# Kernel optimization log

Measured on AMD Instinct MI355X. Metric: run time of the kernel, lower is better.

## Reference

```python
import jax, jax.numpy as jnp
import numpy as np

V = 32000   # src and trg vocab
E = 512     # embed_dim
H = 1024    # hidden_dim
S = 512     # source length
T = 512     # target length


def _lstm_scan(x_seq, h0, c0, Wih, Whh, bih, bhh):
    """Single-layer LSTM over x_seq [L, E] with PyTorch gate order (i,f,g,o)."""
    def step(carry, x):
        h, c = carry
        gates = x @ Wih.T + bih + h @ Whh.T + bhh  # [4H]
        i, f, g, o = jnp.split(gates, 4)
        i = jax.nn.sigmoid(i)
        f = jax.nn.sigmoid(f)
        g = jnp.tanh(g)
        o = jax.nn.sigmoid(o)
        c = f * c + i * g
        h = o * jnp.tanh(c)
        return (h, c), h
    (h, c), hs = jax.lax.scan(step, (h0, c0), x_seq)
    return hs, (h, c)


def setup_inputs() -> dict:
    key = jax.random.key(0)
    ks = jax.random.split(key, 16)
    s = 0.05
    return {
        "source": jax.random.randint(ks[0], (S,), 0, V),
        "target": jax.random.randint(ks[1], (T,), 0, V),
        # encoder params (embed init uniform(-0.25, 0.25) per source)
        "enc_embed": jax.random.uniform(ks[2], (V, E), jnp.float32, -0.25, 0.25),
        "enc_Wih": jax.random.normal(ks[3], (4 * H, E), jnp.float32) * s,
        "enc_Whh": jax.random.normal(ks[4], (4 * H, H), jnp.float32) * s,
        "enc_bih": jnp.zeros((4 * H,), jnp.float32),
        "enc_bhh": jnp.zeros((4 * H,), jnp.float32),
        # decoder params
        "dec_embed": jax.random.normal(ks[5], (V, E), jnp.float32) * s,
        "dec_Wih": jax.random.normal(ks[6], (4 * H, E), jnp.float32) * s,
        "dec_Whh": jax.random.normal(ks[7], (4 * H, H), jnp.float32) * s,
        "dec_bih": jnp.zeros((4 * H,), jnp.float32),
        "dec_bhh": jnp.zeros((4 * H,), jnp.float32),
        "Wout": jax.random.normal(ks[8], (V, H), jnp.float32) * s,
        "bout": jnp.zeros((V,), jnp.float32),
    }


def reference(source, target, enc_embed, enc_Wih, enc_Whh, enc_bih, enc_bhh,
              dec_embed, dec_Wih, dec_Whh, dec_bih, dec_bhh, Wout, bout):
    # ---- encoder: embed source, run LSTM from zero state, take last h ----
    src_emb = enc_embed[source]                       # [S, E]
    h0 = jnp.zeros((H,), src_emb.dtype)
    c0 = jnp.zeros((H,), src_emb.dtype)
    _, (enc_h, _) = _lstm_scan(src_emb, h0, c0, enc_Wih, enc_Whh, enc_bih, enc_bhh)
    # hidden = (enc_h, tanh(enc_h)) as in original forward
    dh0, dc0 = enc_h, jnp.tanh(enc_h)
    # ---- decoder: teacher-forced over target tokens ----
    trg_emb = dec_embed[target]                       # [T, E]
    hs, _ = _lstm_scan(trg_emb, dh0, dc0, dec_Wih, dec_Whh, dec_bih, dec_bhh)  # [T, H]
    logits = hs @ Wout.T + bout                       # [T, V]
    logp = jax.nn.log_softmax(logits, axis=-1)
    # per-step CrossEntropyLoss(output, target[i]) -> list of T scalar losses
    losses = -jnp.take_along_axis(logp, target[:, None], axis=1)[:, 0]  # [T]
    return losses
```

## Files before the change

### kernel.cpp

```cpp
#include <hip/hip_runtime.h>
#include <cstdint>
#include <cstddef>

#define V_ 32000
#define E_ 512
#define H_ 1024
#define S_ 512
#define T_ 512
#define G4 4096

typedef unsigned long long u64;

__device__ __forceinline__ float sigm(float x) { return 1.0f / (1.0f + expf(-x)); }

__global__ __launch_bounds__(256) void xi_gemm(
    const float* __restrict__ emb, const int* __restrict__ tok,
    const float* __restrict__ Wih, const float* __restrict__ b1,
    const float* __restrict__ b2, float* __restrict__ Xi) {
  __shared__ float As[32][68];
  __shared__ float Bs[32][68];
  __shared__ int ids[64];
  const int tid = threadIdx.x;
  const int tx = tid & 15, ty = tid >> 4;
  const int t0 = blockIdx.y * 64, r0 = blockIdx.x * 64;
  if (tid < 64) ids[tid] = tok[t0 + tid];
  __syncthreads();
  const int lrow = tid >> 2;
  const int lk   = (tid & 3) * 8;
  const long arow = (long)ids[lrow] * E_;
  const long brow = (long)(r0 + lrow) * E_;
  float acc[4][4] = {};
  for (int k0 = 0; k0 < E_; k0 += 32) {
    float4 a0 = *(const float4*)(emb + arow + k0 + lk);
    float4 a1 = *(const float4*)(emb + arow + k0 + lk + 4);
    float4 w0 = *(const float4*)(Wih + brow + k0 + lk);
    float4 w1 = *(const float4*)(Wih + brow + k0 + lk + 4);
    __syncthreads();
    As[lk + 0][lrow] = a0.x; As[lk + 1][lrow] = a0.y; As[lk + 2][lrow] = a0.z; As[lk + 3][lrow] = a0.w;
    As[lk + 4][lrow] = a1.x; As[lk + 5][lrow] = a1.y; As[lk + 6][lrow] = a1.z; As[lk + 7][lrow] = a1.w;
    Bs[lk + 0][lrow] = w0.x; Bs[lk + 1][lrow] = w0.y; Bs[lk + 2][lrow] = w0.z; Bs[lk + 3][lrow] = w0.w;
    Bs[lk + 4][lrow] = w1.x; Bs[lk + 5][lrow] = w1.y; Bs[lk + 6][lrow] = w1.z; Bs[lk + 7][lrow] = w1.w;
    __syncthreads();
#pragma unroll
    for (int kk = 0; kk < 32; ++kk) {
      float4 av = *(const float4*)&As[kk][ty * 4];
      float4 bv = *(const float4*)&Bs[kk][tx * 4];
      float a_[4] = {av.x, av.y, av.z, av.w};
      float b_[4] = {bv.x, bv.y, bv.z, bv.w};
#pragma unroll
      for (int i = 0; i < 4; ++i)
#pragma unroll
        for (int j = 0; j < 4; ++j) acc[i][j] += a_[i] * b_[j];
    }
  }
#pragma unroll
  for (int i = 0; i < 4; ++i) {
    const int t = t0 + ty * 4 + i;
#pragma unroll
    for (int j = 0; j < 4; ++j) {
      const int r = r0 + tx * 4 + j;
      Xi[(size_t)t * G4 + r] = acc[i][j] + b1[r] + b2[r];
    }
  }
}

__global__ __launch_bounds__(1024, 4) void lstm_seq(
    const float* __restrict__ Xi_enc, const float* __restrict__ Xi_dec,
    const float* __restrict__ Whh_enc, const float* __restrict__ Whh_dec,
    u64* __restrict__ hpair,
    float* __restrict__ hs) {
  __shared__ float h_lds[16 * 68 + 4];
  __shared__ float gates_lds[64];
  const int tid = threadIdx.x;
  const int wg = blockIdx.x;
  const int r = tid >> 4;
  const int c = tid & 15;
  const int gate = r >> 4, uu = r & 15;
  const int grow = gate * H_ + wg * 16 + uu;
  const int c64 = c * 64;

  float4 w[16];
  {
    const float* wp = Whh_enc + (size_t)grow * H_ + c64;
#pragma unroll
    for (int q = 0; q < 16; ++q) w[q] = *(const float4*)(wp + q * 4);
  }
  const float* Xi = Xi_enc;
  float cstate = 0.f, h_own = 0.f;
  int dead = 0;

  for (int s = 0; s < 1024; ++s) {
    if (s == 512) {
      const float* wp = Whh_dec + (size_t)grow * H_ + c64;
#pragma unroll
      for (int q = 0; q < 16; ++q) w[q] = *(const float4*)(wp + q * 4);
      Xi = Xi_dec;
      if (tid < 16) cstate = tanhf(h_own);
    }
    float xi = 0.f;
    if (c == 0) xi = Xi[(size_t)(s & 511) * G4 + grow];

    const u64* pbase = hpair + (size_t)(s & 1) * H_;
    const unsigned want = (unsigned)s;

    u64 p = __hip_atomic_load(pbase + tid, __ATOMIC_RELAXED, __HIP_MEMORY_SCOPE_AGENT);

    if (tid < 64) {
      const u64* fp = pbase + tid * 16;
      int tries = 0;
      for (;;) {
        u64 f = __hip_atomic_load(fp, __ATOMIC_RELAXED, __HIP_MEMORY_SCOPE_AGENT);
        bool ok = ((int)((unsigned)(f >> 32) - want)) >= 0;
        if (__ballot(ok) == ~0ull) break;
        if (++tries > (1 << 20)) break;
        __builtin_amdgcn_s_sleep(1);
      }
    }
    __syncthreads();

    if ((unsigned)(p >> 32) != want) {
      int tries = 0;
      do {
        p = __hip_atomic_load(pbase + tid, __ATOMIC_RELAXED, __HIP_MEMORY_SCOPE_AGENT);
        if (++tries > (1 << 20)) { dead = 1; break; }
      } while ((unsigned)(p >> 32) != want && !dead);
    }
    h_lds[(tid >> 6) * 68 + (tid & 63)] = __uint_as_float((unsigned)p);
    __syncthreads();

    float acc = 0.f;
    const float* hb = &h_lds[c * 68];
#pragma unroll
    for (int q = 0; q < 16; ++q) {
      float4 h4 = *(const float4*)(hb + q * 4);
      acc += w[q].x * h4.x + w[q].y * h4.y + w[q].z * h4.z + w[q].w * h4.w;
    }
    acc += __shfl_xor(acc, 8, 64);
    acc += __shfl_xor(acc, 4, 64);
    acc += __shfl_xor(acc, 2, 64);
    acc += __shfl_xor(acc, 1, 64);
    if (c == 0) gates_lds[r] = acc + xi;
    __syncthreads();

    if (tid < 16) {
      float ai = gates_lds[tid];
      float af = gates_lds[16 + tid];
      float ag = gates_lds[32 + tid];
      float ao = gates_lds[48 + tid];
      float i_ = sigm(ai), f_ = sigm(af), g_ = tanhf(ag), o_ = sigm(ao);
      cstate = f_ * cstate + i_ * g_;
      float h = o_ * tanhf(cstate);
      h_own = h;
      const int k = wg * 16 + tid;
      u64 pair = ((u64)(unsigned)(s + 1) << 32) | (u64)__float_as_uint(h);
      __hip_atomic_store(hpair + (size_t)((s + 1) & 1) * H_ + k, pair,
                         __ATOMIC_RELAXED, __HIP_MEMORY_SCOPE_AGENT);
      if (s >= 512) hs[(size_t)(s - 512) * H_ + k] = h;
    }
  }
}

#define PHYS(j) ((j) + (((j) >> 5) << 2))

__global__ __launch_bounds__(256) void logits_lse(
    const float* __restrict__ hs, const float* __restrict__ Wout,
    const float* __restrict__ bout, const int* __restrict__ tgt,
    float* __restrict__ pmax, float* __restrict__ psum,
    float* __restrict__ tgtlog) {
  __shared__ float As[32][140];
  __shared__ float Bs[32][140];
  __shared__ float red[128][17];
  __shared__ float Mlds[128];
  __shared__ int tg[128];
  const int tid = threadIdx.x;
  const int tx = tid & 15, ty = tid >> 4;
  const int t0 = blockIdx.y * 128, v0 = blockIdx.x * 128;
  if (tid < 128) tg[tid] = tgt[t0 + tid];
  const int lrow = tid >> 1;
  const int lk   = (tid & 1) * 16;
  const float* ap = hs + (size_t)(t0 + lrow) * H_ + lk;
  const float* bp = Wout + (size_t)(v0 + lrow) * H_ + lk;
  const int pl = PHYS(lrow);
  const int aoff = PHYS(ty * 8);
  const int boff = PHYS(tx * 8);
  float acc[8][8] = {};
  for (int k0 = 0; k0 < H_; k0 += 32) {
    float4 a[4], b[4];
#pragma unroll
    for (int q = 0; q < 4; ++q) {
      a[q] = *(const float4*)(ap + k0 + q * 4);
      b[q] = *(const float4*)(bp + k0 + q * 4);
    }
    __syncthreads();
#pragma unroll
    for (int q = 0; q < 4; ++q) {
      As[lk + q * 4 + 0][pl] = a[q].x; As[lk + q * 4 + 1][pl] = a[q].y;
      As[lk + q * 4 + 2][pl] = a[q].z; As[lk + q * 4 + 3][pl] = a[q].w;
      Bs[lk + q * 4 + 0][pl] = b[q].x; Bs[lk + q * 4 + 1][pl] = b[q].y;
      Bs[lk + q * 4 + 2][pl] = b[q].z; Bs[lk + q * 4 + 3][pl] = b[q].w;
    }
    __syncthreads();
#pragma unroll
    for (int kk = 0; kk < 32; ++kk) {
      float av[8], bv[8];
      *(float4*)&av[0] = *(const float4*)&As[kk][aoff];
      *(float4*)&av[4] = *(const float4*)&As[kk][aoff + 4];
      *(float4*)&bv[0] = *(const float4*)&Bs[kk][boff];
      *(float4*)&bv[4] = *(const float4*)&Bs[kk][boff + 4];
#pragma unroll
      for (int i = 0; i < 8; ++i)
#pragma unroll
        for (int j = 0; j < 8; ++j) acc[i][j] += av[i] * bv[j];
    }
  }
  float bv8[8];
#pragma unroll
  for (int j = 0; j < 8; ++j) bv8[j] = bout[v0 + tx * 8 + j];
#pragma unroll
  for (int i = 0; i < 8; ++i) {
    float m = -3.0e38f;
#pragma unroll
    for (int j = 0; j < 8; ++j) {
      acc[i][j] += bv8[j];
      m = fmaxf(m, acc[i][j]);
    }
    red[ty * 8 + i][tx] = m;
  }
  __syncthreads();
  if (tid < 128) {
    float M = -3.0e38f;
#pragma unroll
    for (int x = 0; x < 16; ++x) M = fmaxf(M, red[tid][x]);
    Mlds[tid] = M;
  }
  __syncthreads();
#pragma unroll
  for (int i = 0; i < 8; ++i) {
    float M = Mlds[ty * 8 + i];
    float ssum = 0.f;
#pragma unroll
    for (int j = 0; j < 8; ++j) ssum += expf(acc[i][j] - M);
    red[ty * 8 + i][tx] = ssum;
  }
  __syncthreads();
  if (tid < 128) {
    float S = 0.f;
#pragma unroll
    for (int x = 0; x < 16; ++x) S += red[tid][x];
    pmax[(size_t)(t0 + tid) * 250 + blockIdx.x] = Mlds[tid];
    psum[(size_t)(t0 + tid) * 250 + blockIdx.x] = S;
  }
#pragma unroll
  for (int i = 0; i < 8; ++i) {
    const int t = t0 + ty * 8 + i;
    const int loc = tg[ty * 8 + i] - v0 - tx * 8;
    if (loc >= 0 && loc < 8) {
#pragma unroll
      for (int j = 0; j < 8; ++j)
        if (j == loc) tgtlog[t] = acc[i][j];
    }
  }
}

__global__ __launch_bounds__(256) void reduce_loss(
    const float* __restrict__ pmax, const float* __restrict__ psum,
    const float* __restrict__ tgtlog, float* __restrict__ out) {
  __shared__ float sm[256];
  __shared__ float ss[256];
  const int t = blockIdx.x, tid = threadIdx.x;
  float m = -3.0e38f;
  if (tid < 250) m = pmax[(size_t)t * 250 + tid];
  sm[tid] = m;
  __syncthreads();
  for (int s = 128; s > 0; s >>= 1) {
    if (tid < s) sm[tid] = fmaxf(sm[tid], sm[tid + s]);
    __syncthreads();
  }
  const float M = sm[0];
  float sv = 0.f;
  if (tid < 250) sv = psum[(size_t)t * 250 + tid] * expf(m - M);
  ss[tid] = sv;
  __syncthreads();
  for (int s = 128; s > 0; s >>= 1) {
    if (tid < s) ss[tid] += ss[tid + s];
    __syncthreads();
  }
  if (tid == 0) out[t] = M + logf(ss[0]) - tgtlog[t];
}

extern "C" void kernel_launch(void* const* d_in, const int* in_sizes, int n_in,
                              void* d_out, int out_size, void* d_ws, size_t ws_size,
                              hipStream_t stream) {
  const int*   source    = (const int*)  d_in[0];
  const int*   target    = (const int*)  d_in[1];
  const float* enc_embed = (const float*)d_in[2];
  const float* enc_Wih   = (const float*)d_in[3];
  const float* enc_Whh   = (const float*)d_in[4];
  const float* enc_bih   = (const float*)d_in[5];
  const float* enc_bhh   = (const float*)d_in[6];
  const float* dec_embed = (const float*)d_in[7];
  const float* dec_Wih   = (const float*)d_in[8];
  const float* dec_Whh   = (const float*)d_in[9];
  const float* dec_bih   = (const float*)d_in[10];
  const float* dec_bhh   = (const float*)d_in[11];
  const float* Wout      = (const float*)d_in[12];
  const float* bout      = (const float*)d_in[13];
  float* out = (float*)d_out;

  char* ws = (char*)d_ws;
  float* Xi_enc = (float*)(ws);
  float* Xi_dec = (float*)(ws + 8388608);
  float* hs     = (float*)(ws + 16777216);
  u64*   hpair  = (u64*)  (ws + 18874368);
  float* pmax   = (float*)(ws + 18890752);
  float* psum   = (float*)(ws + 19402752);
  float* tgtlog = (float*)(ws + 19914752);

  hipMemsetAsync((void*)hpair, 0, 2 * H_ * sizeof(u64), stream);
  xi_gemm<<<dim3(64, 8), 256, 0, stream>>>(enc_embed, source, enc_Wih, enc_bih, enc_bhh, Xi_enc);
  xi_gemm<<<dim3(64, 8), 256, 0, stream>>>(dec_embed, target, dec_Wih, dec_bih, dec_bhh, Xi_dec);
  lstm_seq<<<64, 1024, 0, stream>>>(Xi_enc, Xi_dec, enc_Whh, dec_Whh, hpair, hs);
  logits_lse<<<dim3(250, 4), 256, 0, stream>>>(hs, Wout, bout, target, pmax, psum, tgtlog);
  reduce_loss<<<512, 256, 0, stream>>>(pmax, psum, tgtlog, out);
}
```

Baseline: 3.043 ms.

## Remap LSTM rows so each wave owns one unit, drop block barriers

Remaps the persistent LSTM kernel so each wavefront holds the four gate rows of one hidden unit. The gate nonlinearities can then be gathered with shuffles, with no LDS round trip and two fewer __syncthreads per step. The h buffer in LDS is double-buffered, and every thread spins on its own h element instead of one wave polling for the whole block. Sigmoid and tanh now use hardware exp2 and reciprocal approximations, which trades a little accuracy for shorter latency on the sequential critical path.

Measured after the change: 4.685 ms. 1.54x slower.

```diff
diff --git a/kernel.cpp b/kernel.cpp
--- a/kernel.cpp
+++ b/kernel.cpp
@@ -11,7 +11,13 @@
 
 typedef unsigned long long u64;
 
-__device__ __forceinline__ float sigm(float x) { return 1.0f / (1.0f + expf(-x)); }
+__device__ __forceinline__ float fexp2(float x) { return __builtin_amdgcn_exp2f(x); }
+__device__ __forceinline__ float sigm(float x) {
+  return __builtin_amdgcn_rcpf(1.0f + fexp2(x * -1.442695041f));
+}
+__device__ __forceinline__ float ftanh(float x) {
+  return 2.0f * __builtin_amdgcn_rcpf(1.0f + fexp2(x * -2.885390082f)) - 1.0f;
+}
 
 __global__ __launch_bounds__(256) void xi_gemm(
     const float* __restrict__ emb, const int* __restrict__ tok,
@@ -69,14 +75,15 @@
     const float* __restrict__ Whh_enc, const float* __restrict__ Whh_dec,
     u64* __restrict__ hpair,
     float* __restrict__ hs) {
-  __shared__ float h_lds[16 * 68 + 4];
-  __shared__ float gates_lds[64];
+  __shared__ float h_lds[2][16 * 68 + 4];
   const int tid = threadIdx.x;
   const int wg = blockIdx.x;
-  const int r = tid >> 4;
-  const int c = tid & 15;
-  const int gate = r >> 4, uu = r & 15;
-  const int grow = gate * H_ + wg * 16 + uu;
+  const int wv = tid >> 6;
+  const int ln = tid & 63;
+  const int g  = ln >> 4;
+  const int c  = ln & 15;
+  const int unit = wg * 16 + wv;
+  const int grow = g * H_ + unit;
   const int c64 = c * 64;
 
   float4 w[16];
@@ -95,41 +102,29 @@
 #pragma unroll
       for (int q = 0; q < 16; ++q) w[q] = *(const float4*)(wp + q * 4);
       Xi = Xi_dec;
-      if (tid < 16) cstate = tanhf(h_own);
+      cstate = ftanh(h_own);
     }
     float xi = 0.f;
     if (c == 0) xi = Xi[(size_t)(s & 511) * G4 + grow];
 
-    const u64* pbase = hpair + (size_t)(s & 1) * H_;
+    const u64* pb = hpair + (size_t)(s & 1) * H_;
     const unsigned want = (unsigned)s;
-
-    u64 p = __hip_atomic_load(pbase + tid, __ATOMIC_RELAXED, __HIP_MEMORY_SCOPE_AGENT);
-
-    if (tid < 64) {
-      const u64* fp = pbase + tid * 16;
+    u64 p;
+    {
       int tries = 0;
       for (;;) {
-        u64 f = __hip_atomic_load(fp, __ATOMIC_RELAXED, __HIP_MEMORY_SCOPE_AGENT);
-        bool ok = ((int)((unsigned)(f >> 32) - want)) >= 0;
-        if (__ballot(ok) == ~0ull) break;
-        if (++tries > (1 << 20)) break;
+        p = __hip_atomic_load(pb + tid, __ATOMIC_RELAXED, __HIP_MEMORY_SCOPE_AGENT);
+        if ((unsigned)(p >> 32) == want || dead) break;
+        if (++tries > (1 << 20)) { dead = 1; break; }
         __builtin_amdgcn_s_sleep(1);
       }
     }
-    __syncthreads();
-
-    if ((unsigned)(p >> 32) != want) {
-      int tries = 0;
-      do {
-        p = __hip_atomic_load(pbase + tid, __ATOMIC_RELAXED, __HIP_MEMORY_SCOPE_AGENT);
-        if (++tries > (1 << 20)) { dead = 1; break; }
-      } while ((unsigned)(p >> 32) != want && !dead);
-    }
-    h_lds[(tid >> 6) * 68 + (tid & 63)] = __uint_as_float((unsigned)p);
+    float* buf = h_lds[s & 1];
+    buf[(tid >> 6) * 68 + (tid & 63)] = __uint_as_float((unsigned)p);
     __syncthreads();
 
     float acc = 0.f;
-    const float* hb = &h_lds[c * 68];
+    const float* hb = &buf[c * 68];
 #pragma unroll
     for (int q = 0; q < 16; ++q) {
       float4 h4 = *(const float4*)(hb + q * 4);
@@ -139,23 +134,21 @@
     acc += __shfl_xor(acc, 4, 64);
     acc += __shfl_xor(acc, 2, 64);
     acc += __shfl_xor(acc, 1, 64);
-    if (c == 0) gates_lds[r] = acc + xi;
-    __syncthreads();
-
-    if (tid < 16) {
-      float ai = gates_lds[tid];
-      float af = gates_lds[16 + tid];
-      float ag = gates_lds[32 + tid];
-      float ao = gates_lds[48 + tid];
-      float i_ = sigm(ai), f_ = sigm(af), g_ = tanhf(ag), o_ = sigm(ao);
-      cstate = f_ * cstate + i_ * g_;
-      float h = o_ * tanhf(cstate);
-      h_own = h;
-      const int k = wg * 16 + tid;
+    float val = acc + xi;
+
+    float ai = __shfl(val, 0, 64);
+    float af = __shfl(val, 16, 64);
+    float ag = __shfl(val, 32, 64);
+    float ao = __shfl(val, 48, 64);
+    float i_ = sigm(ai), f_ = sigm(af), g_ = ftanh(ag), o_ = sigm(ao);
+    cstate = f_ * cstate + i_ * g_;
+    float h = o_ * ftanh(cstate);
+    h_own = h;
+    if (ln == 0) {
       u64 pair = ((u64)(unsigned)(s + 1) << 32) | (u64)__float_as_uint(h);
-      __hip_atomic_store(hpair + (size_t)((s + 1) & 1) * H_ + k, pair,
+      __hip_atomic_store(hpair + (size_t)((s + 1) & 1) * H_ + unit, pair,
                          __ATOMIC_RELAXED, __HIP_MEMORY_SCOPE_AGENT);
-      if (s >= 512) hs[(size_t)(s - 512) * H_ + k] = h;
+      if (s >= 512) hs[(size_t)(s - 512) * H_ + unit] = h;
     }
   }
 }
```
